# Optimization experiments

Hardware: AMD Instinct MI355X
Metric: run time of the kernel (lower is better)

Reference implementation:

```python
import jax, jax.numpy as jnp
import numpy as np

T = 4096        # tokens
HC = 4          # hc_mult
HID = 4096      # hidden_size
MAX_IT = 20     # max_sk_it (nested: MAX_IT*MAX_IT inner iterations)
EPS = 1e-12


def setup_inputs() -> dict:
    key = jax.random.key(0)
    k1, k2, k3, k4 = jax.random.split(key, 4)
    out_dim = 2 * HC + HC * HC  # 24
    x = jax.random.normal(k1, (T, HC, HID), dtype=jnp.float32)
    weight = jax.random.normal(k2, (HC * HID, out_dim), dtype=jnp.float32) * 0.02
    bias = jax.random.normal(k3, (out_dim,), dtype=jnp.float32) * 0.02
    alpha = 1.0 + 0.1 * jax.random.normal(k4, (3,), dtype=jnp.float32)
    return {"x": x, "weight": weight, "bias": bias, "alpha": alpha}


def reference(x, weight, bias, alpha):
    t, hc, hid = x.shape
    xf = x.reshape(t, hc * hid)
    # RMSNorm scale absorbed into weight; only 1/rms applied explicitly
    r_inv = jax.lax.rsqrt(jnp.mean(xf * xf, axis=-1, keepdims=True))  # [t,1]
    h = xf.astype(jnp.float32) @ weight  # [t, 2*hc + hc*hc]
    h_pre = h[:, :hc]
    h_post = h[:, hc:2 * hc]
    h_res = h[:, 2 * hc:]
    h_pre = jax.nn.sigmoid(r_inv * alpha[0] * h_pre + bias[:hc])
    h_post = 2.0 * jax.nn.sigmoid(r_inv * alpha[1] * h_post + bias[hc:2 * hc])
    h_res_exp = jnp.exp((r_inv * alpha[2] * h_res + bias[2 * hc:]).reshape(t, hc, hc))

    # Sinkhorn-Knopp: original runs max_it outer x max_it inner identical updates
    u0 = jnp.ones((t, hc), jnp.float32)
    v0 = jnp.ones((t, hc), jnp.float32)

    def step(carry, _):
        u, v = carry
        uv = jnp.einsum('tij,tj->ti', h_res_exp, v)
        u = 1.0 / (uv + EPS)
        vu = jnp.einsum('tij,ti->tj', h_res_exp, u)
        v = 1.0 / (vu + EPS)
        return (u, v), None

    (u, v), _ = jax.lax.scan(step, (u0, v0), None, length=MAX_IT * MAX_IT)
    h_res_out = u[:, :, None] * h_res_exp * v[:, None, :]  # [t,hc,hc]
    return h_pre, h_post, h_res_out
```

## Files before the change

### kernel.cpp

```cpp
#include <hip/hip_runtime.h>
#include <hip/hip_bf16.h>


#define TROWS 4096
#define KDIM  16384
#define NOUT  24
#define RG    128
#define KC    32
#define KPER  (KDIM / KC)
#define TILEK 64
#define NTILE (KPER / TILEK)
#define XSTR  (RG + 1)

__device__ __forceinline__ float fast_rcp(float x)   { return __builtin_amdgcn_rcpf(x); }
__device__ __forceinline__ float fast_rsqrt(float x) { return __builtin_amdgcn_rsqf(x); }

__global__ __launch_bounds__(256) void gemv_part(const float* __restrict__ x,
                                                 const float* __restrict__ w,
                                                 float* __restrict__ hacc) {
    __shared__ float xT[TILEK * XSTR];
    __shared__ float wt[TILEK * NOUT];

    const int bid  = blockIdx.x;
    const int rb   = bid & 31;
    const int kc   = bid >> 5;
    const int rg0  = rb * RG;
    const int k0   = kc * KPER;

    const int t    = threadIdx.x;
    const int wv   = t >> 6;
    const int lane = t & 63;

    const int srow = t >> 4;
    const int sf4  = t & 15;
    const int kk   = sf4 * 4;

    float accA[NOUT + 1], accB[NOUT + 1];
#pragma unroll
    for (int j = 0; j <= NOUT; ++j) { accA[j] = 0.0f; accB[j] = 0.0f; }

    const float* xg = x + (size_t)rg0 * KDIM + k0;

    float4 px[8];
    float4 pw0, pw1;
    {
#pragma unroll
        for (int s = 0; s < 8; ++s)
            px[s] = *(const float4*)(xg + (size_t)(srow + 16 * s) * KDIM + kk);
        const float4* wg4 = (const float4*)(w + (size_t)k0 * NOUT);
        pw0 = wg4[t];
        pw1 = (t < 128) ? wg4[256 + t] : pw0;
    }

#pragma unroll 1
    for (int tile = 0; tile < NTILE; ++tile) {
        __syncthreads();
#pragma unroll
        for (int s = 0; s < 8; ++s) {
            const int row = srow + 16 * s;
            xT[(kk + 0) * XSTR + row] = px[s].x;
            xT[(kk + 1) * XSTR + row] = px[s].y;
            xT[(kk + 2) * XSTR + row] = px[s].z;
            xT[(kk + 3) * XSTR + row] = px[s].w;
        }
        ((float4*)wt)[t] = pw0;
        if (t < 128) ((float4*)wt)[256 + t] = pw1;
        __syncthreads();

        const int tn = (tile + 1 < NTILE) ? tile + 1 : tile;
        const int ktn = tn * TILEK;
#pragma unroll
        for (int s = 0; s < 8; ++s)
            px[s] = *(const float4*)(xg + (size_t)(srow + 16 * s) * KDIM + ktn + kk);
        {
            const float4* wg4 = (const float4*)(w + (size_t)(k0 + ktn) * NOUT);
            pw0 = wg4[t];
            pw1 = (t < 128) ? wg4[256 + t] : pw0;
        }

        const float* xk = xT + (wv * 16) * XSTR;
        const float* wk = wt + (wv * 16) * NOUT;
#pragma unroll
        for (int u = 0; u < 16; ++u) {
            const float xa = xk[u * XSTR + lane];
            const float xb = xk[u * XSTR + 64 + lane];
            const float4* wr = (const float4*)(wk + u * NOUT);
            float wbuf[24];
            *(float4*)(wbuf +  0) = wr[0];
            *(float4*)(wbuf +  4) = wr[1];
            *(float4*)(wbuf +  8) = wr[2];
            *(float4*)(wbuf + 12) = wr[3];
            *(float4*)(wbuf + 16) = wr[4];
            *(float4*)(wbuf + 20) = wr[5];
            accA[NOUT] = fmaf(xa, xa, accA[NOUT]);
            accB[NOUT] = fmaf(xb, xb, accB[NOUT]);
#pragma unroll
            for (int j = 0; j < NOUT; ++j) {
                accA[j] = fmaf(wbuf[j], xa, accA[j]);
                accB[j] = fmaf(wbuf[j], xb, accB[j]);
            }
        }
    }

#pragma unroll
    for (int j = 0; j <= NOUT; ++j) {
        atomicAdd(hacc + (size_t)j * TROWS + rg0 + lane,      accA[j]);
        atomicAdd(hacc + (size_t)j * TROWS + rg0 + 64 + lane, accB[j]);
    }
}

__global__ __launch_bounds__(64) void sinkhorn_epilogue(const float* __restrict__ hacc,
                                                        const float* __restrict__ bias,
                                                        const float* __restrict__ alpha,
                                                        float* __restrict__ out) {
    const int row = blockIdx.x * 64 + threadIdx.x;

    float h[25];
#pragma unroll
    for (int j = 0; j < 25; ++j) h[j] = hacc[(size_t)j * TROWS + row];

    const float r_inv = fast_rsqrt(h[24] * (1.0f / (float)KDIM));
    const float a0 = alpha[0], a1 = alpha[1], a2 = alpha[2];

#pragma unroll
    for (int i = 0; i < 4; ++i) {
        const float zpre = fmaf(r_inv * a0, h[i], bias[i]);
        out[(size_t)row * 4 + i] = fast_rcp(1.0f + __expf(-zpre));
        const float zpo = fmaf(r_inv * a1, h[4 + i], bias[4 + i]);
        out[(size_t)16384 + (size_t)row * 4 + i] = 2.0f * fast_rcp(1.0f + __expf(-zpo));
    }

    float E[16];
#pragma unroll
    for (int t = 0; t < 16; ++t)
        E[t] = __expf(fmaf(r_inv * a2, h[8 + t], bias[8 + t]));

    float u0 = 1.0f, u1 = 1.0f, u2 = 1.0f, u3 = 1.0f;
    float v0 = 1.0f, v1 = 1.0f, v2 = 1.0f, v3 = 1.0f;

#pragma unroll 1
    for (int it = 0; it < 400; ++it) {
        float s0 = fmaf(E[0],  v0, fmaf(E[1],  v1, fmaf(E[2],  v2, E[3]  * v3)));
        float s1 = fmaf(E[4],  v0, fmaf(E[5],  v1, fmaf(E[6],  v2, E[7]  * v3)));
        float s2 = fmaf(E[8],  v0, fmaf(E[9],  v1, fmaf(E[10], v2, E[11] * v3)));
        float s3 = fmaf(E[12], v0, fmaf(E[13], v1, fmaf(E[14], v2, E[15] * v3)));
        u0 = fast_rcp(s0 + 1e-12f);
        u1 = fast_rcp(s1 + 1e-12f);
        u2 = fast_rcp(s2 + 1e-12f);
        u3 = fast_rcp(s3 + 1e-12f);
        float t0 = fmaf(E[0], u0, fmaf(E[4], u1, fmaf(E[8],  u2, E[12] * u3)));
        float t1 = fmaf(E[1], u0, fmaf(E[5], u1, fmaf(E[9],  u2, E[13] * u3)));
        float t2 = fmaf(E[2], u0, fmaf(E[6], u1, fmaf(E[10], u2, E[14] * u3)));
        float t3 = fmaf(E[3], u0, fmaf(E[7], u1, fmaf(E[11], u2, E[15] * u3)));
        v0 = fast_rcp(t0 + 1e-12f);
        v1 = fast_rcp(t1 + 1e-12f);
        v2 = fast_rcp(t2 + 1e-12f);
        v3 = fast_rcp(t3 + 1e-12f);
    }

    const size_t ob = 32768 + (size_t)row * 16;
    out[ob + 0]  = u0 * E[0]  * v0;
    out[ob + 1]  = u0 * E[1]  * v1;
    out[ob + 2]  = u0 * E[2]  * v2;
    out[ob + 3]  = u0 * E[3]  * v3;
    out[ob + 4]  = u1 * E[4]  * v0;
    out[ob + 5]  = u1 * E[5]  * v1;
    out[ob + 6]  = u1 * E[6]  * v2;
    out[ob + 7]  = u1 * E[7]  * v3;
    out[ob + 8]  = u2 * E[8]  * v0;
    out[ob + 9]  = u2 * E[9]  * v1;
    out[ob + 10] = u2 * E[10] * v2;
    out[ob + 11] = u2 * E[11] * v3;
    out[ob + 12] = u3 * E[12] * v0;
    out[ob + 13] = u3 * E[13] * v1;
    out[ob + 14] = u3 * E[14] * v2;
    out[ob + 15] = u3 * E[15] * v3;
}

extern "C" void kernel_launch(void* const* d_in, const int* in_sizes, int n_in,
                              void* d_out, int out_size, void* d_ws, size_t ws_size,
                              hipStream_t stream) {
    const float* x     = (const float*)d_in[0];
    const float* w     = (const float*)d_in[1];
    const float* bias  = (const float*)d_in[2];
    const float* alpha = (const float*)d_in[3];
    float* out  = (float*)d_out;
    float* hacc = (float*)d_ws;

    hipMemsetAsync(hacc, 0, (size_t)(NOUT + 1) * TROWS * sizeof(float), stream);
    gemv_part<<<dim3(32 * KC), dim3(256), 0, stream>>>(x, w, hacc);
    sinkhorn_epilogue<<<dim3(TROWS / 64), dim3(64), 0, stream>>>(hacc, bias, alpha, out);
}
```

Baseline: 446.0 us.

## Restructure GEMV tiling with swizzled double buffer, split-K partials, and Sinkhorn early exit

The GEMV kernel now handles 256 rows per block with a K tile of 32. It keeps x in a swizzled row-major double buffer in shared memory instead of a transposed copy, and each thread accumulates 4 rows. Partial results are reduced inside the block with shared-memory atomics and written as per-K-chunk partials with no global atomics, so the memset goes away. The epilogue then sums the 32 partials. The Sinkhorn loop uses a shallower FMA tree and exits early once the whole wavefront's u and v stop changing bitwise, which cuts iterations but adds a compare each step and can change rounding slightly.

```diff
diff --git a/kernel.cpp b/kernel.cpp
--- a/kernel.cpp
+++ b/kernel.cpp
@@ -1,16 +1,14 @@
 #include <hip/hip_runtime.h>
-#include <hip/hip_bf16.h>
 
 
 #define TROWS 4096
 #define KDIM  16384
 #define NOUT  24
-#define RG    128
+#define RG    256
 #define KC    32
 #define KPER  (KDIM / KC)
-#define TILEK 64
+#define TILEK 32
 #define NTILE (KPER / TILEK)
-#define XSTR  (RG + 1)
 
 __device__ __forceinline__ float fast_rcp(float x)   { return __builtin_amdgcn_rcpf(x); }
 __device__ __forceinline__ float fast_rsqrt(float x) { return __builtin_amdgcn_rsqf(x); }
@@ -18,94 +16,119 @@
 __global__ __launch_bounds__(256) void gemv_part(const float* __restrict__ x,
                                                  const float* __restrict__ w,
                                                  float* __restrict__ hacc) {
-    __shared__ float xT[TILEK * XSTR];
-    __shared__ float wt[TILEK * NOUT];
+    __shared__ float4 xb[2][RG * TILEK / 4];
+    __shared__ float4 wb[2][TILEK * NOUT / 4];
 
     const int bid  = blockIdx.x;
-    const int rb   = bid & 31;
-    const int kc   = bid >> 5;
+    const int rb   = bid & 15;
+    const int kc   = bid >> 4;
     const int rg0  = rb * RG;
     const int k0   = kc * KPER;
 
     const int t    = threadIdx.x;
     const int wv   = t >> 6;
     const int lane = t & 63;
-
-    const int srow = t >> 4;
-    const int sf4  = t & 15;
-    const int kk   = sf4 * 4;
-
-    float accA[NOUT + 1], accB[NOUT + 1];
-#pragma unroll
-    for (int j = 0; j <= NOUT; ++j) { accA[j] = 0.0f; accB[j] = 0.0f; }
+    const int xorl = lane & 7;
+
+    float acc[4][NOUT + 1];
+#pragma unroll
+    for (int c = 0; c < 4; ++c)
+#pragma unroll
+        for (int j = 0; j <= NOUT; ++j) acc[c][j] = 0.0f;
 
     const float* xg = x + (size_t)rg0 * KDIM + k0;
 
     float4 px[8];
-    float4 pw0, pw1;
-    {
-#pragma unroll
-        for (int s = 0; s < 8; ++s)
-            px[s] = *(const float4*)(xg + (size_t)(srow + 16 * s) * KDIM + kk);
-        const float4* wg4 = (const float4*)(w + (size_t)k0 * NOUT);
-        pw0 = wg4[t];
-        pw1 = (t < 128) ? wg4[256 + t] : pw0;
-    }
-
+    float4 pw;
+
+    auto loadT = [&](int kt) {
+#pragma unroll
+        for (int s = 0; s < 8; ++s) {
+            const int q = t + 256 * s;
+            px[s] = *(const float4*)(xg + (size_t)(q >> 3) * KDIM + kt + 4 * (q & 7));
+        }
+        if (t < 192) pw = *(const float4*)(w + (size_t)(k0 + kt) * NOUT + 4 * t);
+    };
+    auto writeT = [&](int pn) {
+#pragma unroll
+        for (int s = 0; s < 8; ++s) {
+            const int q   = t + 256 * s;
+            const int row = q >> 3;
+            const int g   = q & 7;
+            xb[pn][row * 8 + (g ^ (row & 7))] = px[s];
+        }
+        if (t < 192) wb[pn][t] = pw;
+    };
+
+    loadT(0);
+    writeT(0);
+    __syncthreads();
+
+    int p = 0;
 #pragma unroll 1
     for (int tile = 0; tile < NTILE; ++tile) {
-        __syncthreads();
-#pragma unroll
-        for (int s = 0; s < 8; ++s) {
-            const int row = srow + 16 * s;
-            xT[(kk + 0) * XSTR + row] = px[s].x;
-            xT[(kk + 1) * XSTR + row] = px[s].y;
-            xT[(kk + 2) * XSTR + row] = px[s].z;
-            xT[(kk + 3) * XSTR + row] = px[s].w;
-        }
-        ((float4*)wt)[t] = pw0;
-        if (t < 128) ((float4*)wt)[256 + t] = pw1;
-        __syncthreads();
-
-        const int tn = (tile + 1 < NTILE) ? tile + 1 : tile;
-        const int ktn = tn * TILEK;
-#pragma unroll
-        for (int s = 0; s < 8; ++s)
-            px[s] = *(const float4*)(xg + (size_t)(srow + 16 * s) * KDIM + ktn + kk);
-        {
-            const float4* wg4 = (const float4*)(w + (size_t)(k0 + ktn) * NOUT);
-            pw0 = wg4[t];
-            pw1 = (t < 128) ? wg4[256 + t] : pw0;
-        }
-
-        const float* xk = xT + (wv * 16) * XSTR;
-        const float* wk = wt + (wv * 16) * NOUT;
-#pragma unroll
-        for (int u = 0; u < 16; ++u) {
-            const float xa = xk[u * XSTR + lane];
-            const float xb = xk[u * XSTR + 64 + lane];
-            const float4* wr = (const float4*)(wk + u * NOUT);
-            float wbuf[24];
-            *(float4*)(wbuf +  0) = wr[0];
-            *(float4*)(wbuf +  4) = wr[1];
-            *(float4*)(wbuf +  8) = wr[2];
-            *(float4*)(wbuf + 12) = wr[3];
-            *(float4*)(wbuf + 16) = wr[4];
-            *(float4*)(wbuf + 20) = wr[5];
-            accA[NOUT] = fmaf(xa, xa, accA[NOUT]);
-            accB[NOUT] = fmaf(xb, xb, accB[NOUT]);
-#pragma unroll
-            for (int j = 0; j < NOUT; ++j) {
-                accA[j] = fmaf(wbuf[j], xa, accA[j]);
-                accB[j] = fmaf(wbuf[j], xb, accB[j]);
+        const bool more = (tile + 1 < NTILE);
+        if (more) loadT((tile + 1) * TILEK);
+
+        const float4* xp = xb[p];
+        const float*  wp = (const float*)wb[p];
+#pragma unroll
+        for (int gg = 0; gg < 2; ++gg) {
+            const int u4 = 2 * wv + gg;
+            float4 xv[4];
+#pragma unroll
+            for (int c = 0; c < 4; ++c)
+                xv[c] = xp[(lane + 64 * c) * 8 + (u4 ^ xorl)];
+#pragma unroll
+            for (int kk = 0; kk < 4; ++kk) {
+                const float4* wr = (const float4*)(wp + (u4 * 4 + kk) * NOUT);
+                float wf[NOUT];
+                *(float4*)(wf +  0) = wr[0];
+                *(float4*)(wf +  4) = wr[1];
+                *(float4*)(wf +  8) = wr[2];
+                *(float4*)(wf + 12) = wr[3];
+                *(float4*)(wf + 16) = wr[4];
+                *(float4*)(wf + 20) = wr[5];
+                const float x0 = kk == 0 ? xv[0].x : kk == 1 ? xv[0].y : kk == 2 ? xv[0].z : xv[0].w;
+                const float x1 = kk == 0 ? xv[1].x : kk == 1 ? xv[1].y : kk == 2 ? xv[1].z : xv[1].w;
+                const float x2 = kk == 0 ? xv[2].x : kk == 1 ? xv[2].y : kk == 2 ? xv[2].z : xv[2].w;
+                const float x3 = kk == 0 ? xv[3].x : kk == 1 ? xv[3].y : kk == 2 ? xv[3].z : xv[3].w;
+                acc[0][NOUT] = fmaf(x0, x0, acc[0][NOUT]);
+                acc[1][NOUT] = fmaf(x1, x1, acc[1][NOUT]);
+                acc[2][NOUT] = fmaf(x2, x2, acc[2][NOUT]);
+                acc[3][NOUT] = fmaf(x3, x3, acc[3][NOUT]);
+#pragma unroll
+                for (int j = 0; j < NOUT; ++j) {
+                    acc[0][j] = fmaf(wf[j], x0, acc[0][j]);
+                    acc[1][j] = fmaf(wf[j], x1, acc[1][j]);
+                    acc[2][j] = fmaf(wf[j], x2, acc[2][j]);
+                    acc[3][j] = fmaf(wf[j], x3, acc[3][j]);
+                }
             }
         }
-    }
-
-#pragma unroll
-    for (int j = 0; j <= NOUT; ++j) {
-        atomicAdd(hacc + (size_t)j * TROWS + rg0 + lane,      accA[j]);
-        atomicAdd(hacc + (size_t)j * TROWS + rg0 + 64 + lane, accB[j]);
+
+        if (more) writeT(p ^ 1);
+        __syncthreads();
+        p ^= 1;
+    }
+
+    float* lacc = (float*)xb;
+#pragma unroll 1
+    for (int i = t; i < 25 * RG; i += 256) lacc[i] = 0.0f;
+    __syncthreads();
+#pragma unroll
+    for (int c = 0; c < 4; ++c) {
+        const int row = lane + 64 * c;
+#pragma unroll
+        for (int j = 0; j <= NOUT; ++j)
+            atomicAdd(&lacc[j * RG + row], acc[c][j]);
+    }
+    __syncthreads();
+#pragma unroll 1
+    for (int i = t; i < 25 * RG; i += 256) {
+        const int j = i >> 8;
+        const int r = i & 255;
+        hacc[((size_t)kc * 25 + j) * TROWS + rg0 + r] = lacc[i];
     }
 }
 
@@ -117,7 +140,13 @@
 
     float h[25];
 #pragma unroll
-    for (int j = 0; j < 25; ++j) h[j] = hacc[(size_t)j * TROWS + row];
+    for (int j = 0; j < 25; ++j) h[j] = 0.0f;
+#pragma unroll 1
+    for (int c = 0; c < KC; ++c) {
+        const float* hp = hacc + (size_t)c * 25 * TROWS + row;
+#pragma unroll
+        for (int j = 0; j < 25; ++j) h[j] += hp[(size_t)j * TROWS];
+    }
 
     const float r_inv = fast_rsqrt(h[24] * (1.0f / (float)KDIM));
     const float a0 = alpha[0], a1 = alpha[1], a2 = alpha[2];
@@ -132,30 +161,38 @@
 
     float E[16];
 #pragma unroll
-    for (int t = 0; t < 16; ++t)
-        E[t] = __expf(fmaf(r_inv * a2, h[8 + t], bias[8 + t]));
+    for (int q = 0; q < 16; ++q)
+        E[q] = __expf(fmaf(r_inv * a2, h[8 + q], bias[8 + q]));
 
     float u0 = 1.0f, u1 = 1.0f, u2 = 1.0f, u3 = 1.0f;
     float v0 = 1.0f, v1 = 1.0f, v2 = 1.0f, v3 = 1.0f;
+    float pu0 = 1.0f, pu1 = 1.0f, pu2 = 1.0f, pu3 = 1.0f;
+    float pv0 = 1.0f, pv1 = 1.0f, pv2 = 1.0f, pv3 = 1.0f;
 
 #pragma unroll 1
     for (int it = 0; it < 400; ++it) {
-        float s0 = fmaf(E[0],  v0, fmaf(E[1],  v1, fmaf(E[2],  v2, E[3]  * v3)));
-        float s1 = fmaf(E[4],  v0, fmaf(E[5],  v1, fmaf(E[6],  v2, E[7]  * v3)));
-        float s2 = fmaf(E[8],  v0, fmaf(E[9],  v1, fmaf(E[10], v2, E[11] * v3)));
-        float s3 = fmaf(E[12], v0, fmaf(E[13], v1, fmaf(E[14], v2, E[15] * v3)));
+        float s0 = fmaf(E[0],  v0, E[1]  * v1) + fmaf(E[2],  v2, E[3]  * v3);
+        float s1 = fmaf(E[4],  v0, E[5]  * v1) + fmaf(E[6],  v2, E[7]  * v3);
+        float s2 = fmaf(E[8],  v0, E[9]  * v1) + fmaf(E[10], v2, E[11] * v3);
+        float s3 = fmaf(E[12], v0, E[13] * v1) + fmaf(E[14], v2, E[15] * v3);
         u0 = fast_rcp(s0 + 1e-12f);
         u1 = fast_rcp(s1 + 1e-12f);
         u2 = fast_rcp(s2 + 1e-12f);
         u3 = fast_rcp(s3 + 1e-12f);
-        float t0 = fmaf(E[0], u0, fmaf(E[4], u1, fmaf(E[8],  u2, E[12] * u3)));
-        float t1 = fmaf(E[1], u0, fmaf(E[5], u1, fmaf(E[9],  u2, E[13] * u3)));
-        float t2 = fmaf(E[2], u0, fmaf(E[6], u1, fmaf(E[10], u2, E[14] * u3)));
-        float t3 = fmaf(E[3], u0, fmaf(E[7], u1, fmaf(E[11], u2, E[15] * u3)));
+        float t0 = fmaf(E[0], u0, E[4]  * u1) + fmaf(E[8],  u2, E[12] * u3);
+        float t1 = fmaf(E[1], u0, E[5]  * u1) + fmaf(E[9],  u2, E[13] * u3);
+        float t2 = fmaf(E[2], u0, E[6]  * u1) + fmaf(E[10], u2, E[14] * u3);
+        float t3 = fmaf(E[3], u0, E[7]  * u1) + fmaf(E[11], u2, E[15] * u3);
         v0 = fast_rcp(t0 + 1e-12f);
         v1 = fast_rcp(t1 + 1e-12f);
         v2 = fast_rcp(t2 + 1e-12f);
         v3 = fast_rcp(t3 + 1e-12f);
+
+        const int conv = (u0 == pu0) & (u1 == pu1) & (u2 == pu2) & (u3 == pu3)
+                       & (v0 == pv0) & (v1 == pv1) & (v2 == pv2) & (v3 == pv3);
+        pu0 = u0; pu1 = u1; pu2 = u2; pu3 = u3;
+        pv0 = v0; pv1 = v1; pv2 = v2; pv3 = v3;
+        if (__all(conv)) break;
     }
 
     const size_t ob = 32768 + (size_t)row * 16;
@@ -187,7 +224,6 @@
     float* out  = (float*)d_out;
     float* hacc = (float*)d_ws;
 
-    hipMemsetAsync(hacc, 0, (size_t)(NOUT + 1) * TROWS * sizeof(float), stream);
-    gemv_part<<<dim3(32 * KC), dim3(256), 0, stream>>>(x, w, hacc);
+    gemv_part<<<dim3((TROWS / RG) * KC), dim3(256), 0, stream>>>(x, w, hacc);
     sinkhorn_epilogue<<<dim3(TROWS / 64), dim3(64), 0, stream>>>(hacc, bias, alpha, out);
 }
```

Measured after the change: 596.5 us. 1.34x slower.
